# Optimization experiments

Measured on AMD Instinct MI355X. Metric: run time of the kernel, lower is better.

Reference implementation:

```python
import jax, jax.numpy as jnp
import numpy as np

B, IN_F, OUT_F = 1024, 512, 512


def setup_inputs() -> dict:
    key = jax.random.key(0)
    k1, k2 = jax.random.split(key)
    x = jax.random.uniform(k1, (B, IN_F), dtype=jnp.float32)
    weight = jax.random.uniform(k2, (IN_F, OUT_F), dtype=jnp.float32)
    return {"x": x, "weight": weight}


def reference(x, weight):
    # Max-min fuzzy composition (tropical semiring 'matmul'):
    # out[b, o] = max_i min(x[b, i], W[i, o])
    # x: [B, IN], weight: [IN, OUT] -> out: [B, OUT]
    return jnp.max(jnp.minimum(x[:, :, None], weight[None, :, :]), axis=1)
```

## Files before the change

### kernel.cpp

```cpp
#include <hip/hip_runtime.h>


typedef unsigned int u32;
typedef u32 u32x2 __attribute__((ext_vector_type(2)));
typedef u32 u32x4 __attribute__((ext_vector_type(4)));
typedef float f4 __attribute__((ext_vector_type(4)));
typedef float f2 __attribute__((ext_vector_type(2)));
typedef __fp16 h2 __attribute__((ext_vector_type(2)));

#define XB 8192
#define WB 16384
#define BUFB (XB + WB)

static __device__ __forceinline__ u32 pkcvt(float a, float b) {
  return __builtin_bit_cast(u32, __builtin_amdgcn_cvt_pkrtz(a, b));
}
static __device__ __forceinline__ u32 pkmax(u32 a, u32 b) {
  u32 d; asm("v_pk_max_u16 %0, %1, %2" : "=v"(d) : "v"(a), "v"(b)); return d;
}
static __device__ __forceinline__ u32 pkmin_bl(u32 x, u32 w) {
  u32 d;
  asm("v_pk_min_u16 %0, %1, %2 op_sel:[0,0] op_sel_hi:[0,1]"
      : "=v"(d) : "v"(x), "v"(w));
  return d;
}
static __device__ __forceinline__ u32 pkmin_bh(u32 x, u32 w) {
  u32 d;
  asm("v_pk_min_u16 %0, %1, %2 op_sel:[1,0] op_sel_hi:[1,1]"
      : "=v"(d) : "v"(x), "v"(w));
  return d;
}

__global__ __launch_bounds__(1024, 4) void maxmin_v5(const float* __restrict__ X,
                                                     const float* __restrict__ W,
                                                     float* __restrict__ Out) {
  __shared__ __align__(16) char smem[65536];

  const int tid  = threadIdx.x;
  const int wv   = tid >> 6;
  const int lane = tid & 63;
  const int ty   = lane >> 3;
  const int tx   = lane & 7;
  const int b0   = blockIdx.x * 32;
  const int o0   = blockIdx.y * 64;

  const int xr  = tid >> 5;
  const int xkq = tid & 31;
  const float* xg = X + (b0 + xr) * 512 + xkq * 4;
  const int xw0 = (2 * xkq) * 128 + 4 * (xr ^ ((2 * xkq) & 28));

  const int wkk = tid >> 4;
  const int wc4 = tid & 15;
  const float* wg = W + wkk * 512 + o0 + wc4 * 4;
  const int ww0 = XB + wkk * 128 + wc4 * 8;

  const int xro = 16 * (ty ^ (wv & 7));
  const int wro = XB + 16 * tx;

  u32 acc[4][4] = {};

  auto stage = [&](char* buf, f4 xv, f4 wa, f4 wb) {
    *(u32*)(buf + xw0)       = pkcvt(xv.x, xv.y);
    *(u32*)(buf + xw0 + 128) = pkcvt(xv.z, xv.w);
    u32x2 wpa = {pkcvt(wa.x, wa.y), pkcvt(wa.z, wa.w)};
    *(u32x2*)(buf + ww0) = wpa;
    u32x2 wpb = {pkcvt(wb.x, wb.y), pkcvt(wb.z, wb.w)};
    *(u32x2*)(buf + ww0 + 64 * 128) = wpb;
  };

  {
    f4 xv = *(const f4*)xg;
    f4 wa = *(const f4*)wg;
    f4 wb = *(const f4*)(wg + 64 * 512);
    stage(smem, xv, wa, wb);
  }
  __syncthreads();

  for (int c = 0; c < 4; ++c) {
    f4 nx = {}, na = {}, nb = {};
    if (c < 3) {
      nx = *(const f4*)(xg + (c + 1) * 128);
      na = *(const f4*)(wg + (c + 1) * 128 * 512);
      nb = *(const f4*)(wg + (c + 1) * 128 * 512 + 64 * 512);
    }
    const char* buf = smem + (c & 1) * BUFB;
#pragma unroll
    for (int q = 0; q < 4; ++q) {
      const int kp = 4 * wv + q;
      u32x4 xv = *(const u32x4*)(buf + kp * 128 + xro);
      u32x4 wl = *(const u32x4*)(buf + wro + (2 * kp) * 128);
      u32x4 wh = *(const u32x4*)(buf + wro + (2 * kp + 1) * 128);
#pragma unroll
      for (int j = 0; j < 4; ++j)
#pragma unroll
        for (int cc = 0; cc < 4; ++cc) {
          acc[j][cc] = pkmax(acc[j][cc], pkmin_bl(xv[j], wl[cc]));
          acc[j][cc] = pkmax(acc[j][cc], pkmin_bh(xv[j], wh[cc]));
        }
    }
    if (c < 3) stage(smem + ((c + 1) & 1) * BUFB, nx, na, nb);
    __syncthreads();
  }

#pragma unroll
  for (int j = 0; j < 4; ++j) {
    u32x4 v = {acc[j][0], acc[j][1], acc[j][2], acc[j][3]};
    *(u32x4*)(smem + wv * 4096 + (4 * ty + j) * 128 + tx * 16) = v;
  }
  __syncthreads();

  const int row = tid >> 5;
  const int cp  = tid & 31;
  const int cb  = row * 128 + cp * 4;
  u32 m = *(const u32*)(smem + cb);
#pragma unroll
  for (int g = 1; g < 16; ++g) m = pkmax(m, *(const u32*)(smem + g * 4096 + cb));
  h2 hm = __builtin_bit_cast(h2, m);
  f2 o = {(float)hm.x, (float)hm.y};
  *(f2*)(Out + (b0 + row) * 512 + o0 + cp * 2) = o;
}

extern "C" void kernel_launch(void* const* d_in, const int* in_sizes, int n_in,
                              void* d_out, int out_size, void* d_ws, size_t ws_size,
                              hipStream_t stream) {
  const float* x = (const float*)d_in[0];
  const float* w = (const float*)d_in[1];
  float* out = (float*)d_out;
  (void)in_sizes; (void)n_in; (void)out_size; (void)d_ws; (void)ws_size;
  dim3 grid(1024 / 32, 512 / 64);
  maxmin_v5<<<grid, 1024, 0, stream>>>(x, w, out);
}
```

Before: 66.98 us.

## Give each thread an 8x4 tile and split k across wave halves

Each thread now holds 8 rows by 4 column-pairs of packed fp16 accumulators instead of 4x4. The two halves of each wave take different k-pairs, each running half as many k iterations. This reuses each loaded W vector across twice as many X rows, which cuts LDS reads per min/max operation. The two half-wave partial maxima are merged with v_permlane32_swap before the cross-wave LDS reduction. The cost is roughly double the accumulator registers, which may strain occupancy under launch_bounds(1024,4), and the X LDS addressing now uses a different swizzle.

```diff
diff --git a/kernel.cpp b/kernel.cpp
--- a/kernel.cpp
+++ b/kernel.cpp
@@ -30,8 +30,13 @@
       : "=v"(d) : "v"(x), "v"(w));
   return d;
 }
+static __device__ __forceinline__ u32 halfswap_max(u32 v) {
+  u32 a = v, b = v;
+  asm("v_permlane32_swap_b32 %0, %1" : "+v"(a), "+v"(b));
+  return pkmax(a, b);
+}
 
-__global__ __launch_bounds__(1024, 4) void maxmin_v5(const float* __restrict__ X,
+__global__ __launch_bounds__(1024, 4) void maxmin_v6(const float* __restrict__ X,
                                                      const float* __restrict__ W,
                                                      float* __restrict__ Out) {
   __shared__ __align__(16) char smem[65536];
@@ -39,8 +44,10 @@
   const int tid  = threadIdx.x;
   const int wv   = tid >> 6;
   const int lane = tid & 63;
-  const int ty   = lane >> 3;
-  const int tx   = lane & 7;
+  const int sh   = lane >> 5;
+  const int l5   = lane & 31;
+  const int ty   = l5 >> 3;
+  const int tx   = l5 & 7;
   const int b0   = blockIdx.x * 32;
   const int o0   = blockIdx.y * 64;
 
@@ -54,10 +61,10 @@
   const float* wg = W + wkk * 512 + o0 + wc4 * 4;
   const int ww0 = XB + wkk * 128 + wc4 * 8;
 
-  const int xro = 16 * (ty ^ (wv & 7));
+  const int kpb = 4 * wv + 2 * sh;
   const int wro = XB + 16 * tx;
 
-  u32 acc[4][4] = {};
+  u32 acc[8][4] = {};
 
   auto stage = [&](char* buf, f4 xv, f4 wa, f4 wb) {
     *(u32*)(buf + xw0)       = pkcvt(xv.x, xv.y);
@@ -85,17 +92,21 @@
     }
     const char* buf = smem + (c & 1) * BUFB;
 #pragma unroll
-    for (int q = 0; q < 4; ++q) {
-      const int kp = 4 * wv + q;
-      u32x4 xv = *(const u32x4*)(buf + kp * 128 + xro);
+    for (int q = 0; q < 2; ++q) {
+      const int kp = kpb + q;
+      const int m  = kp & 28;
+      u32x4 x0 = *(const u32x4*)(buf + kp * 128 + 4 * ((8 * ty) ^ m));
+      u32x4 x1 = *(const u32x4*)(buf + kp * 128 + 4 * ((8 * ty + 4) ^ m));
       u32x4 wl = *(const u32x4*)(buf + wro + (2 * kp) * 128);
-      u32x4 wh = *(const u32x4*)(buf + wro + (2 * kp + 1) * 128);
+      u32x4 wh = *(const u32x4*)(buf + wro + (2 * kp) * 128 + 128);
 #pragma unroll
       for (int j = 0; j < 4; ++j)
 #pragma unroll
         for (int cc = 0; cc < 4; ++cc) {
-          acc[j][cc] = pkmax(acc[j][cc], pkmin_bl(xv[j], wl[cc]));
-          acc[j][cc] = pkmax(acc[j][cc], pkmin_bh(xv[j], wh[cc]));
+          acc[j][cc]     = pkmax(acc[j][cc],     pkmin_bl(x0[j], wl[cc]));
+          acc[j][cc]     = pkmax(acc[j][cc],     pkmin_bh(x0[j], wh[cc]));
+          acc[4 + j][cc] = pkmax(acc[4 + j][cc], pkmin_bl(x1[j], wl[cc]));
+          acc[4 + j][cc] = pkmax(acc[4 + j][cc], pkmin_bh(x1[j], wh[cc]));
         }
     }
     if (c < 3) stage(smem + ((c + 1) & 1) * BUFB, nx, na, nb);
@@ -103,9 +114,16 @@
   }
 
 #pragma unroll
-  for (int j = 0; j < 4; ++j) {
-    u32x4 v = {acc[j][0], acc[j][1], acc[j][2], acc[j][3]};
-    *(u32x4*)(smem + wv * 4096 + (4 * ty + j) * 128 + tx * 16) = v;
+  for (int j = 0; j < 8; ++j)
+#pragma unroll
+    for (int cc = 0; cc < 4; ++cc) acc[j][cc] = halfswap_max(acc[j][cc]);
+
+  if (sh == 0) {
+#pragma unroll
+    for (int j = 0; j < 8; ++j) {
+      u32x4 v = {acc[j][0], acc[j][1], acc[j][2], acc[j][3]};
+      *(u32x4*)(smem + wv * 4096 + (8 * ty + j) * 128 + tx * 16) = v;
+    }
   }
   __syncthreads();
 
@@ -128,5 +146,5 @@
   float* out = (float*)d_out;
   (void)in_sizes; (void)n_in; (void)out_size; (void)d_ws; (void)ws_size;
   dim3 grid(1024 / 32, 512 / 64);
-  maxmin_v5<<<grid, 1024, 0, stream>>>(x, w, out);
+  maxmin_v6<<<grid, 1024, 0, stream>>>(x, w, out);
 }
```

Result: no change. 67.87 us (+1.3%).
